# Kernel tuning notes

Measured on AMD Instinct MI355X. Metric: run time of the kernel, lower is better.

Reference implementation:

```python
import jax, jax.numpy as jnp
import numpy as np

B, S, H = 32, 4096, 1024


def setup_inputs() -> dict:
    key = jax.random.key(0)
    k1, k2 = jax.random.split(key)
    lstm_outputs = jax.random.normal(k1, (B, S, H), dtype=jnp.float32)
    w_attn = jax.random.normal(k2, (H,), dtype=jnp.float32) * (1.0 / np.sqrt(H))
    return {"lstm_outputs": lstm_outputs, "w_attn": w_attn}


def reference(lstm_outputs, w_attn):
    # energy: [B, S] = tanh(lstm_outputs @ w)
    energy = jnp.tanh(jnp.einsum("bsh,h->bs", lstm_outputs, w_attn))
    attn = jax.nn.softmax(energy, axis=1)  # softmax over sequence dim
    # context: [B, H] weighted sum over sequence
    context = jnp.einsum("bs,bsh->bh", attn, lstm_outputs)
    return context
```

## Files before the change

kernel.cpp:

```cpp
#include <hip/hip_runtime.h>
#include <math.h>

#define BB 32
#define SS 4096
#define HH 1024
#define CHUNKS 32
#define ROWS_PER_BLOCK (SS / CHUNKS)
#define WAVES 4
#define ROWS_PER_WAVE (ROWS_PER_BLOCK / WAVES)
#define U 8

__device__ __forceinline__ float softmax_w(float s) {
    float t  = __expf(2.0f * s);
    float th = 1.0f - 2.0f * __builtin_amdgcn_rcpf(t + 1.0f);
    return __expf(th);
}

__global__ __launch_bounds__(256, 2) void attn_pass1(
    const float* __restrict__ x, const float* __restrict__ w,
    float* __restrict__ pc, float* __restrict__ pl)
{
    const int tid  = threadIdx.x;
    const int wave = tid >> 6;
    const int lane = tid & 63;
    const int blk  = blockIdx.x;
    const int b    = blk / CHUNKS;
    const int chunk= blk % CHUNKS;

    const float* xb = x + (long long)b * SS * HH
                        + (long long)chunk * ROWS_PER_BLOCK * HH
                        + (long long)wave * ROWS_PER_WAVE * HH
                        + lane * 4;

    float4 wv[4];
#pragma unroll
    for (int k = 0; k < 4; ++k)
        wv[k] = *(const float4*)(w + k * 256 + lane * 4);

    float4 acc[4];
#pragma unroll
    for (int k = 0; k < 4; ++k) acc[k] = make_float4(0.f, 0.f, 0.f, 0.f);
    float l = 0.f;

#pragma unroll 1
    for (int r = 0; r < ROWS_PER_WAVE; r += U) {
        const float* xr = xb + (long long)r * HH;

        float4 v[U][4];
#pragma unroll
        for (int u = 0; u < U; ++u)
#pragma unroll
            for (int k = 0; k < 4; ++k)
                v[u][k] = *(const float4*)(xr + (long long)u * HH + k * 256);

        float t[U];
#pragma unroll
        for (int u = 0; u < U; ++u) t[u] = 0.f;
#pragma unroll
        for (int k = 0; k < 4; ++k)
#pragma unroll
            for (int u = 0; u < U; ++u) {
                t[u] = fmaf(v[u][k].x, wv[k].x, t[u]);
                t[u] = fmaf(v[u][k].y, wv[k].y, t[u]);
                t[u] = fmaf(v[u][k].z, wv[k].z, t[u]);
                t[u] = fmaf(v[u][k].w, wv[k].w, t[u]);
            }

#pragma unroll
        for (int off = 32; off >= 1; off >>= 1)
#pragma unroll
            for (int u = 0; u < U; ++u)
                t[u] += __shfl_xor(t[u], off, 64);

        float p[U];
#pragma unroll
        for (int u = 0; u < U; ++u) {
            p[u] = softmax_w(t[u]);
            l += p[u];
        }

#pragma unroll
        for (int k = 0; k < 4; ++k)
#pragma unroll
            for (int u = 0; u < U; ++u) {
                acc[k].x = fmaf(p[u], v[u][k].x, acc[k].x);
                acc[k].y = fmaf(p[u], v[u][k].y, acc[k].y);
                acc[k].z = fmaf(p[u], v[u][k].z, acc[k].z);
                acc[k].w = fmaf(p[u], v[u][k].w, acc[k].w);
            }
    }

    __shared__ float lds_c[WAVES * HH];
    __shared__ float lds_l[WAVES];
#pragma unroll
    for (int k = 0; k < 4; ++k)
        *(float4*)(lds_c + wave * HH + k * 256 + lane * 4) = acc[k];
    if (lane == 0) lds_l[wave] = l;
    __syncthreads();

    float4 c = *(const float4*)(lds_c + tid * 4);
#pragma unroll
    for (int wv2 = 1; wv2 < WAVES; ++wv2) {
        float4 o = *(const float4*)(lds_c + wv2 * HH + tid * 4);
        c.x += o.x; c.y += o.y; c.z += o.z; c.w += o.w;
    }
    *(float4*)(pc + (long long)blk * HH + tid * 4) = c;
    if (tid == 0)
        pl[blk] = lds_l[0] + lds_l[1] + lds_l[2] + lds_l[3];
}

__global__ __launch_bounds__(256) void attn_pass2(
    const float* __restrict__ pc, const float* __restrict__ pl,
    float* __restrict__ out)
{
    const int b = blockIdx.x;
    const int t = threadIdx.x;
    float l = 0.f;
    float4 c = make_float4(0.f, 0.f, 0.f, 0.f);
#pragma unroll
    for (int i = 0; i < CHUNKS; ++i) {
        const int blk = b * CHUNKS + i;
        l += pl[blk];
        float4 o = *(const float4*)(pc + (long long)blk * HH + t * 4);
        c.x += o.x; c.y += o.y; c.z += o.z; c.w += o.w;
    }
    const float inv = 1.f / l;
    float4 r = make_float4(c.x * inv, c.y * inv, c.z * inv, c.w * inv);
    *(float4*)(out + (long long)b * HH + t * 4) = r;
}

extern "C" void kernel_launch(void* const* d_in, const int* in_sizes, int n_in,
                              void* d_out, int out_size, void* d_ws, size_t ws_size,
                              hipStream_t stream) {
    const float* x = (const float*)d_in[0];
    const float* w = (const float*)d_in[1];
    float* out = (float*)d_out;

    float* pc = (float*)d_ws;
    float* pl = pc + (size_t)BB * CHUNKS * HH;

    attn_pass1<<<BB * CHUNKS, 256, 0, stream>>>(x, w, pc, pl);
    attn_pass2<<<BB, 256, 0, stream>>>(pc, pl, out);
}
```

Measured before the change: 682.5 us.

## Stream rows through per-wave LDS ring via async global_load_lds prefetch

Replaces the register-batched 8-row loads with a per-wave 4-deep LDS ring filled by direct global-to-LDS loads, prefetching three rows ahead and using explicit vmcnt waits. Each iteration then processes one row read back from LDS with ds_read_b128. The goal is to keep memory requests in flight continuously while cutting register pressure. In exchange it adds an LDS round trip and hand-written waitcnt logic, and it serialises per-row shuffle reductions, which could limit throughput on this bandwidth-bound kernel.

```diff
diff --git a/kernel.cpp b/kernel.cpp
--- a/kernel.cpp
+++ b/kernel.cpp
@@ -1,5 +1,6 @@
 #include <hip/hip_runtime.h>
 #include <math.h>
+#include <stdint.h>
 
 #define BB 32
 #define SS 4096
@@ -8,12 +9,33 @@
 #define ROWS_PER_BLOCK (SS / CHUNKS)
 #define WAVES 4
 #define ROWS_PER_WAVE (ROWS_PER_BLOCK / WAVES)
-#define U 8
+#define NBUF 4
+
+typedef __attribute__((ext_vector_type(4))) float f32x4;
 
 __device__ __forceinline__ float softmax_w(float s) {
     float t  = __expf(2.0f * s);
     float th = 1.0f - 2.0f * __builtin_amdgcn_rcpf(t + 1.0f);
     return __expf(th);
+}
+
+__device__ __forceinline__ unsigned lds_base_off(const void* p) {
+    return (unsigned)(uintptr_t)(__attribute__((address_space(3))) const char*)p;
+}
+
+__device__ __forceinline__ f32x4 lds_read_b128(unsigned byte_off) {
+    f32x4 r;
+    asm volatile("ds_read_b128 %0, %1" : "=&v"(r) : "v"(byte_off));
+    return r;
+}
+
+__device__ __forceinline__ void issue_row(const float* gl, float* lbase) {
+#pragma unroll
+    for (int j = 0; j < 4; ++j)
+        __builtin_amdgcn_global_load_lds(
+            (const __attribute__((address_space(1))) void*)(gl + j * 256),
+            (__attribute__((address_space(3))) void*)(lbase + j * 256),
+            16, 0, 0);
 }
 
 __global__ __launch_bounds__(256, 2) void attn_pass1(
@@ -27,71 +49,88 @@
     const int b    = blk / CHUNKS;
     const int chunk= blk % CHUNKS;
 
-    const float* xb = x + (long long)b * SS * HH
+    __shared__ float smem[WAVES * NBUF * 1024];
+    __shared__ float lds_l[WAVES];
+
+    const float* xw = x + (long long)b * SS * HH
                         + (long long)chunk * ROWS_PER_BLOCK * HH
-                        + (long long)wave * ROWS_PER_WAVE * HH
-                        + lane * 4;
+                        + (long long)wave * ROWS_PER_WAVE * HH;
+    const float* gl = xw + lane * 4;
+    float* ring = smem + wave * (NBUF * 1024);
 
     float4 wv[4];
 #pragma unroll
     for (int k = 0; k < 4; ++k)
         wv[k] = *(const float4*)(w + k * 256 + lane * 4);
+    asm volatile("s_waitcnt vmcnt(0)");
+    __builtin_amdgcn_sched_barrier(0);
+
+#pragma unroll
+    for (int s = 0; s < NBUF - 1; ++s)
+        issue_row(gl + (long long)s * HH, ring + s * 1024);
+    __builtin_amdgcn_sched_barrier(0);
 
     float4 acc[4];
 #pragma unroll
     for (int k = 0; k < 4; ++k) acc[k] = make_float4(0.f, 0.f, 0.f, 0.f);
     float l = 0.f;
 
+    const unsigned ring_off = lds_base_off(ring) + lane * 16;
+
 #pragma unroll 1
-    for (int r = 0; r < ROWS_PER_WAVE; r += U) {
-        const float* xr = xb + (long long)r * HH;
+    for (int r = 0; r < ROWS_PER_WAVE; ++r) {
+        const int buf = r & (NBUF - 1);
 
-        float4 v[U][4];
-#pragma unroll
-        for (int u = 0; u < U; ++u)
-#pragma unroll
-            for (int k = 0; k < 4; ++k)
-                v[u][k] = *(const float4*)(xr + (long long)u * HH + k * 256);
+        if (r + 3 < ROWS_PER_WAVE) {
+            issue_row(gl + (long long)(r + 3) * HH, ring + ((r + 3) & (NBUF - 1)) * 1024);
+            __builtin_amdgcn_sched_barrier(0);
+            asm volatile("s_waitcnt vmcnt(12)");
+        } else if (r == ROWS_PER_WAVE - 3) {
+            asm volatile("s_waitcnt vmcnt(8)");
+        } else if (r == ROWS_PER_WAVE - 2) {
+            asm volatile("s_waitcnt vmcnt(4)");
+        } else {
+            asm volatile("s_waitcnt vmcnt(0)");
+        }
+        __builtin_amdgcn_sched_barrier(0);
 
-        float t[U];
-#pragma unroll
-        for (int u = 0; u < U; ++u) t[u] = 0.f;
-#pragma unroll
-        for (int k = 0; k < 4; ++k)
-#pragma unroll
-            for (int u = 0; u < U; ++u) {
-                t[u] = fmaf(v[u][k].x, wv[k].x, t[u]);
-                t[u] = fmaf(v[u][k].y, wv[k].y, t[u]);
-                t[u] = fmaf(v[u][k].z, wv[k].z, t[u]);
-                t[u] = fmaf(v[u][k].w, wv[k].w, t[u]);
-            }
+        const unsigned base = ring_off + buf * 4096;
+        f32x4 v0 = lds_read_b128(base);
+        f32x4 v1 = lds_read_b128(base + 1024);
+        f32x4 v2 = lds_read_b128(base + 2048);
+        f32x4 v3 = lds_read_b128(base + 3072);
+        asm volatile("s_waitcnt lgkmcnt(0)");
+        __builtin_amdgcn_sched_barrier(0);
+
+        float t = 0.f;
+        t = fmaf(v0.x, wv[0].x, t); t = fmaf(v0.y, wv[0].y, t);
+        t = fmaf(v0.z, wv[0].z, t); t = fmaf(v0.w, wv[0].w, t);
+        t = fmaf(v1.x, wv[1].x, t); t = fmaf(v1.y, wv[1].y, t);
+        t = fmaf(v1.z, wv[1].z, t); t = fmaf(v1.w, wv[1].w, t);
+        t = fmaf(v2.x, wv[2].x, t); t = fmaf(v2.y, wv[2].y, t);
+        t = fmaf(v2.z, wv[2].z, t); t = fmaf(v2.w, wv[2].w, t);
+        t = fmaf(v3.x, wv[3].x, t); t = fmaf(v3.y, wv[3].y, t);
+        t = fmaf(v3.z, wv[3].z, t); t = fmaf(v3.w, wv[3].w, t);
 
 #pragma unroll
         for (int off = 32; off >= 1; off >>= 1)
-#pragma unroll
-            for (int u = 0; u < U; ++u)
-                t[u] += __shfl_xor(t[u], off, 64);
+            t += __shfl_xor(t, off, 64);
 
-        float p[U];
-#pragma unroll
-        for (int u = 0; u < U; ++u) {
-            p[u] = softmax_w(t[u]);
-            l += p[u];
-        }
+        const float p = softmax_w(t);
+        l += p;
 
-#pragma unroll
-        for (int k = 0; k < 4; ++k)
-#pragma unroll
-            for (int u = 0; u < U; ++u) {
-                acc[k].x = fmaf(p[u], v[u][k].x, acc[k].x);
-                acc[k].y = fmaf(p[u], v[u][k].y, acc[k].y);
-                acc[k].z = fmaf(p[u], v[u][k].z, acc[k].z);
-                acc[k].w = fmaf(p[u], v[u][k].w, acc[k].w);
-            }
+        acc[0].x = fmaf(p, v0.x, acc[0].x); acc[0].y = fmaf(p, v0.y, acc[0].y);
+        acc[0].z = fmaf(p, v0.z, acc[0].z); acc[0].w = fmaf(p, v0.w, acc[0].w);
+        acc[1].x = fmaf(p, v1.x, acc[1].x); acc[1].y = fmaf(p, v1.y, acc[1].y);
+        acc[1].z = fmaf(p, v1.z, acc[1].z); acc[1].w = fmaf(p, v1.w, acc[1].w);
+        acc[2].x = fmaf(p, v2.x, acc[2].x); acc[2].y = fmaf(p, v2.y, acc[2].y);
+        acc[2].z = fmaf(p, v2.z, acc[2].z); acc[2].w = fmaf(p, v2.w, acc[2].w);
+        acc[3].x = fmaf(p, v3.x, acc[3].x); acc[3].y = fmaf(p, v3.y, acc[3].y);
+        acc[3].z = fmaf(p, v3.z, acc[3].z); acc[3].w = fmaf(p, v3.w, acc[3].w);
     }
 
-    __shared__ float lds_c[WAVES * HH];
-    __shared__ float lds_l[WAVES];
+    __syncthreads();
+    float* lds_c = smem;
 #pragma unroll
     for (int k = 0; k < 4; ++k)
         *(float4*)(lds_c + wave * HH + k * 256 + lane * 4) = acc[k];
```

After: 676.2 us. About the same (-0.9%).
